# Optimization experiments

Hardware: AMD Instinct MI355X
Metric: run time of the kernel (lower is better)

The kernel has to match this reference:

```python
import jax, jax.numpy as jnp
import numpy as np

BATCH, SEQ, IN, HID = 256, 512, 64, 512


def _xavier(key, shape):
    fan_in, fan_out = shape[1], shape[0]
    limit = float(np.sqrt(6.0 / (fan_in + fan_out)))
    return jax.random.uniform(key, shape, jnp.float32, -limit, limit)


def setup_inputs() -> dict:
    key = jax.random.key(0)
    k1, k2, k3 = jax.random.split(key, 3)
    return {
        "x": jax.random.normal(k1, (BATCH, SEQ, IN), jnp.float32),
        "h0": jnp.zeros((BATCH, HID), jnp.float32),
        "W_ih": _xavier(k2, (HID, IN)),
        "W_hh": _xavier(k3, (HID, HID)),
        "b_ih": jnp.zeros((HID,), jnp.float32),
        "b_hh": jnp.zeros((HID,), jnp.float32),
    }


def reference(x, h0, W_ih, W_hh, b_ih, b_hh):
    # Precompute input projection for all timesteps at once: (B,S,H)
    x_proj = jnp.einsum('bsi,hi->bsh', x, W_ih) + b_ih + b_hh

    def step(h, xp_t):
        h_new = jnp.tanh(xp_t + h @ W_hh.T)  # (B,H)
        return h_new, h_new

    # scan over time axis; xs must be time-major
    h_n, _ = jax.lax.scan(step, h0, jnp.swapaxes(x_proj, 0, 1))
    last_step_features = h_n  # out[:, -1, :] equals final hidden state
    return (last_step_features, h_n)
```

## Files before the change

kernel.cpp:

```cpp
#include <hip/hip_runtime.h>
#include <stdint.h>

#define BATCH 256
#define SEQ   512
#define INDIM 64
#define HID   512

typedef _Float16 half2_t __attribute__((ext_vector_type(2)));

__device__ __forceinline__ float dot2f(uint32_t w, uint32_t h, float acc) {
    return __builtin_amdgcn_fdot2(__builtin_bit_cast(half2_t, w),
                                  __builtin_bit_cast(half2_t, h), acc, false);
}
__device__ __forceinline__ uint32_t pack2(float a, float b) {
    half2_t h; h[0] = (_Float16)a; h[1] = (_Float16)b;
    return __builtin_bit_cast(uint32_t, h);
}
template<int CTRL>
__device__ __forceinline__ float dpp_sum(float x) {
    int xi = __builtin_bit_cast(int, x);
    int yi = __builtin_amdgcn_mov_dpp(xi, CTRL, 0xF, 0xF, true);
    return x + __builtin_bit_cast(float, yi);
}
__device__ __forceinline__ float swz4_sum(float x) {
    int xi = __builtin_bit_cast(int, x);
    int yi = __builtin_amdgcn_ds_swizzle(xi, 0x101F);
    return x + __builtin_bit_cast(float, yi);
}

struct Smem {
    uint4     wl[16][512];
    _Float16  hbuf[2][8][72];
};

#define DOT4(accv, wrow, hc) \
    accv = dot2f((wrow)[0], hc.x, accv); accv = dot2f((wrow)[1], hc.y, accv); \
    accv = dot2f((wrow)[2], hc.z, accv); accv = dot2f((wrow)[3], hc.w, accv);

__global__ __launch_bounds__(512, 2)
void rnn_ksplit_kernel(const float* __restrict__ x,
                       const float* __restrict__ h0,
                       const float* __restrict__ W_ih,
                       const float* __restrict__ W_hh,
                       const float* __restrict__ b_ih,
                       const float* __restrict__ b_hh,
                       float* __restrict__ out)
{
    __shared__ Smem sm;
    const int t = threadIdx.x;
    const int b = blockIdx.x;
    const int s = t & 7;
    const int rbase = t & ~7;

    uint32_t wreg[6][32];
    #pragma unroll
    for (int j = 0; j < 6; ++j) {
        const float* wr = W_hh + (size_t)(rbase + j) * HID + s * 64;
        #pragma unroll
        for (int q = 0; q < 16; ++q) {
            float4 v4 = ((const float4*)wr)[q];
            wreg[j][2*q]   = pack2(v4.x, v4.y);
            wreg[j][2*q+1] = pack2(v4.z, v4.w);
        }
    }
    #pragma unroll
    for (int v = 0; v < 2; ++v) {
        const float* wr = W_hh + (size_t)(rbase + 6 + v) * HID + s * 64;
        #pragma unroll
        for (int c = 0; c < 8; ++c) {
            float4 aa = ((const float4*)wr)[2*c];
            float4 bb = ((const float4*)wr)[2*c+1];
            uint4 wv;
            wv.x = pack2(aa.x, aa.y); wv.y = pack2(aa.z, aa.w);
            wv.z = pack2(bb.x, bb.y); wv.w = pack2(bb.z, bb.w);
            sm.wl[v*8 + c][t] = wv;
        }
    }
    uint32_t wih[8][4];
    #pragma unroll
    for (int j = 0; j < 8; ++j) {
        const float* wr = W_ih + (size_t)(rbase + j) * INDIM + s * 8;
        float4 aa = ((const float4*)wr)[0];
        float4 bb = ((const float4*)wr)[1];
        wih[j][0] = pack2(aa.x, aa.y); wih[j][1] = pack2(aa.z, aa.w);
        wih[j][2] = pack2(bb.x, bb.y); wih[j][3] = pack2(bb.z, bb.w);
    }

    const float bsum = b_ih[t] + b_hh[t];
    sm.hbuf[0][t >> 6][t & 63] = (_Float16)h0[(size_t)b * HID + t];

    const float* xbase = x + (size_t)b * SEQ * INDIM + s * 8;
    float4 xa = ((const float4*)xbase)[0];
    float4 xb = ((const float4*)xbase)[1];

    const bool b0 = (s & 1) != 0, b1 = (s & 2) != 0, b2 = (s & 4) != 0;

    __syncthreads();

    float hlast = 0.f;
    #pragma unroll 1
    for (int tt = 0; tt < SEQ; ++tt) {
        const int tn = (tt + 1 < SEQ) ? tt + 1 : tt;
        const float* xp = xbase + (size_t)tn * INDIM;
        float4 xa_n = ((const float4*)xp)[0];
        float4 xb_n = ((const float4*)xp)[1];

        const int par = tt & 1;
        float a0=0,a1=0,a2=0,a3=0,a4=0,a5=0,a6=0,a7=0;
        const uint4* hp = (const uint4*)&sm.hbuf[par][s][0];

        #pragma unroll
        for (int c = 0; c < 8; ++c) {
            uint4 hc = hp[c];
            uint4 w6 = sm.wl[c][t];
            uint4 w7 = sm.wl[8 + c][t];
            DOT4(a0, &wreg[0][4*c], hc);
            DOT4(a1, &wreg[1][4*c], hc);
            DOT4(a2, &wreg[2][4*c], hc);
            DOT4(a3, &wreg[3][4*c], hc);
            DOT4(a4, &wreg[4][4*c], hc);
            DOT4(a5, &wreg[5][4*c], hc);
            a6 = dot2f(w6.x, hc.x, a6); a6 = dot2f(w6.y, hc.y, a6);
            a6 = dot2f(w6.z, hc.z, a6); a6 = dot2f(w6.w, hc.w, a6);
            a7 = dot2f(w7.x, hc.x, a7); a7 = dot2f(w7.y, hc.y, a7);
            a7 = dot2f(w7.z, hc.z, a7); a7 = dot2f(w7.w, hc.w, a7);
        }

        {
            uint32_t xp0 = pack2(xa.x, xa.y), xp1 = pack2(xa.z, xa.w);
            uint32_t xp2 = pack2(xb.x, xb.y), xp3 = pack2(xb.z, xb.w);
            uint4 xc; xc.x = xp0; xc.y = xp1; xc.z = xp2; xc.w = xp3;
            DOT4(a0, wih[0], xc); DOT4(a1, wih[1], xc);
            DOT4(a2, wih[2], xc); DOT4(a3, wih[3], xc);
            DOT4(a4, wih[4], xc); DOT4(a5, wih[5], xc);
            DOT4(a6, wih[6], xc); DOT4(a7, wih[7], xc);
        }

        float t0 = dpp_sum<0xB1>(a0), u0 = dpp_sum<0xB1>(a1);
        float t1 = dpp_sum<0xB1>(a2), u1 = dpp_sum<0xB1>(a3);
        float t2 = dpp_sum<0xB1>(a4), u2 = dpp_sum<0xB1>(a5);
        float t3 = dpp_sum<0xB1>(a6), u3 = dpp_sum<0xB1>(a7);
        float q0 = b0 ? u0 : t0;
        float q1 = b0 ? u1 : t1;
        float q2 = b0 ? u2 : t2;
        float q3 = b0 ? u3 : t3;
        float r0a = dpp_sum<0x4E>(q0), r0b = dpp_sum<0x4E>(q1);
        float r1a = dpp_sum<0x4E>(q2), r1b = dpp_sum<0x4E>(q3);
        float r0 = b1 ? r0b : r0a;
        float r1 = b1 ? r1b : r1a;
        float f0 = swz4_sum(r0), f1 = swz4_sum(r1);
        float acc = (b2 ? f1 : f0) + bsum;

        float e  = __expf(2.0f * acc);
        float th = 1.0f - 2.0f * __builtin_amdgcn_rcpf(e + 1.0f);

        sm.hbuf[1 - par][t >> 6][t & 63] = (_Float16)th;
        hlast = th;
        xa = xa_n; xb = xb_n;
        __syncthreads();
    }

    out[(size_t)b * HID + t] = hlast;
    out[(size_t)BATCH * HID + (size_t)b * HID + t] = hlast;
}

extern "C" void kernel_launch(void* const* d_in, const int* in_sizes, int n_in,
                              void* d_out, int out_size, void* d_ws, size_t ws_size,
                              hipStream_t stream) {
    (void)in_sizes; (void)n_in; (void)out_size; (void)d_ws; (void)ws_size;
    const float* x    = (const float*)d_in[0];
    const float* h0   = (const float*)d_in[1];
    const float* W_ih = (const float*)d_in[2];
    const float* W_hh = (const float*)d_in[3];
    const float* b_ih = (const float*)d_in[4];
    const float* b_hh = (const float*)d_in[5];
    float* out = (float*)d_out;

    hipLaunchKernelGGL(rnn_ksplit_kernel, dim3(BATCH), dim3(512), 0, stream,
                       x, h0, W_ih, W_hh, b_ih, b_hh, out);
}
```

Before: 962.3 us.

## Rewrite RNN recurrence with MFMA over 16-batch tiles and precomputed input projection

Adds a path that precomputes the input projection for all timesteps with an MFMA GEMM into workspace as fp16. It then runs the recurrence on 16 blocks, each handling 16 batch rows with MFMA 16x16x32. W_hh is split across registers, LDS and a global-memory copy in a pre-swizzled layout. The goal is to replace scalar dot2 work with matrix cores, at the cost of using only 16 CUs, serial latency per step, and a large fp16 workspace. The old kernel remains as a fallback when the workspace is too small.

Measured after the change: 2.628 ms. 173% more time.

```diff
diff --git a/kernel.cpp b/kernel.cpp
--- a/kernel.cpp
+++ b/kernel.cpp
@@ -6,8 +6,222 @@
 #define INDIM 64
 #define HID   512
 
+typedef _Float16 f16;
+typedef _Float16 f16x2 __attribute__((ext_vector_type(2)));
+typedef _Float16 f16x8 __attribute__((ext_vector_type(8)));
+typedef float    f32x4 __attribute__((ext_vector_type(4)));
+
+#define XP_BYTES  134217728ULL
+#define WSC_BYTES 65536ULL
+#define WS_NEED   (XP_BYTES + WSC_BYTES)
+
+__device__ __forceinline__ int row_of(int wv, int rho, int m) {
+    return wv*128 + (rho>>1)*32 + (m>>2)*8 + (rho&1)*4 + (m&3);
+}
+__device__ __forceinline__ f16x2 pkrtz(float a, float b) {
+    return __builtin_bit_cast(f16x2, __builtin_amdgcn_cvt_pkrtz(a, b));
+}
+union FU { f16x8 v; f16x2 h2[4]; uint32_t u[4]; };
+__device__ __forceinline__ f16x8 pack8(float4 a, float4 b) {
+    FU r;
+    r.h2[0] = pkrtz(a.x, a.y); r.h2[1] = pkrtz(a.z, a.w);
+    r.h2[2] = pkrtz(b.x, b.y); r.h2[3] = pkrtz(b.z, b.w);
+    return r.v;
+}
+__device__ __forceinline__ float fast_tanh(float x) {
+    float e = __expf(2.0f * x);
+    return 1.0f - 2.0f * __builtin_amdgcn_rcpf(e + 1.0f);
+}
+__device__ __forceinline__ f32x4 mfma16(f16x8 a, f16x8 b, f32x4 c) {
+    return __builtin_amdgcn_mfma_f32_16x16x32_f16(a, b, c, 0, 0, 0);
+}
+
+__global__ void wconv_kernel(const float* __restrict__ W_hh, f16* __restrict__ wsc)
+{
+    int id = blockIdx.x * 256 + threadIdx.x;
+    if (id >= 2*32*64) return;
+    int l = id & 63, tile = (id >> 6) & 31, ks = id >> 11;
+    int wv = tile >> 3, rho = tile & 7, g = l >> 4, c = l & 15;
+    const float* p = W_hh + (size_t)row_of(wv, rho, c) * HID + (14 + ks) * 32 + g * 8;
+    f16x8 v = pack8(((const float4*)p)[0], ((const float4*)p)[1]);
+    *(f16x8*)(wsc + (size_t)id * 8) = v;
+}
+
+__global__ __launch_bounds__(256)
+void xp_gemm_kernel(const float* __restrict__ x, const float* __restrict__ W_ih,
+                    const float* __restrict__ b_ih, const float* __restrict__ b_hh,
+                    f16* __restrict__ xp)
+{
+    const int t = threadIdx.x, wv = t >> 6, l = t & 63, g = l >> 4, c = l & 15;
+    const int bb = blockIdx.x;
+    const int sc = blockIdx.y;
+
+    f16x8 wf[8][2];
+    #pragma unroll
+    for (int rho = 0; rho < 8; ++rho) {
+        const float* pr = W_ih + (size_t)row_of(wv, rho, c) * INDIM;
+        #pragma unroll
+        for (int kx = 0; kx < 2; ++kx) {
+            const float* p4 = pr + kx * 32 + g * 8;
+            wf[rho][kx] = pack8(((const float4*)p4)[0], ((const float4*)p4)[1]);
+        }
+    }
+    float bias[8][4];
+    #pragma unroll
+    for (int rho = 0; rho < 8; ++rho)
+        #pragma unroll
+        for (int r = 0; r < 4; ++r) {
+            int row = row_of(wv, rho, 4 * g + r);
+            bias[rho][r] = b_ih[row] + b_hh[row];
+        }
+
+    const float* xb = x + (size_t)(bb * 16 + c) * SEQ * INDIM;
+    #pragma unroll 1
+    for (int si = 0; si < 32; ++si) {
+        const int s = sc * 32 + si;
+        const float* xs = xb + (size_t)s * INDIM;
+        f16x8 bx[2];
+        #pragma unroll
+        for (int kx = 0; kx < 2; ++kx) {
+            const float* p4 = xs + kx * 32 + g * 8;
+            bx[kx] = pack8(((const float4*)p4)[0], ((const float4*)p4)[1]);
+        }
+        #pragma unroll
+        for (int rho = 0; rho < 8; ++rho) {
+            f32x4 acc; acc[0] = bias[rho][0]; acc[1] = bias[rho][1];
+            acc[2] = bias[rho][2]; acc[3] = bias[rho][3];
+            acc = mfma16(wf[rho][0], bx[0], acc);
+            acc = mfma16(wf[rho][1], bx[1], acc);
+            f16x2 lo = pkrtz(acc[0], acc[1]), hi = pkrtz(acc[2], acc[3]);
+            uint2 st;
+            st.x = __builtin_bit_cast(uint32_t, lo);
+            st.y = __builtin_bit_cast(uint32_t, hi);
+            size_t idx = (((size_t)bb * SEQ + s) * 32 + wv * 8 + rho) * 64 + l;
+            *(uint2*)(xp + idx * 4) = st;
+        }
+    }
+}
+
+__global__ __launch_bounds__(256, 1)
+void rnn_mfma_kernel(const float* __restrict__ h0, const float* __restrict__ W_hh,
+                     const f16* __restrict__ xp, const f16* __restrict__ wsc,
+                     float* __restrict__ out)
+{
+    __shared__ f16x8 s_wlds[3 * 32 * 64];
+    __shared__ f16x8 s_hbuf[2 * 16 * 64];
+    const int t = threadIdx.x, wv = t >> 6, l = t & 63, g = l >> 4, c = l & 15;
+    const int bb = blockIdx.x;
+
+    f16x8 wreg[11][8];
+    #pragma unroll
+    for (int kk = 0; kk < 11; ++kk)
+        #pragma unroll
+        for (int rho = 0; rho < 8; ++rho) {
+            const float* p4 = W_hh + (size_t)row_of(wv, rho, c) * HID + kk * 32 + g * 8;
+            wreg[kk][rho] = pack8(((const float4*)p4)[0], ((const float4*)p4)[1]);
+        }
+    #pragma unroll
+    for (int kk = 0; kk < 3; ++kk)
+        #pragma unroll
+        for (int rho = 0; rho < 8; ++rho) {
+            const float* p4 = W_hh + (size_t)row_of(wv, rho, c) * HID + (11 + kk) * 32 + g * 8;
+            s_wlds[(kk * 32 + wv * 8 + rho) * 64 + l] =
+                pack8(((const float4*)p4)[0], ((const float4*)p4)[1]);
+        }
+    f16x8 ownf[4];
+    #pragma unroll
+    for (int P = 0; P < 4; ++P) {
+        const float* p4 = h0 + (size_t)(bb * 16 + c) * HID + (4 * wv + P) * 32 + g * 8;
+        ownf[P] = pack8(((const float4*)p4)[0], ((const float4*)p4)[1]);
+        s_hbuf[(4 * wv + P) * 64 + l] = ownf[P];
+    }
+
+    const f16* xpb = xp + ((size_t)bb * SEQ * 32 + wv * 8) * 256;
+    uint2 xn[8];
+    #pragma unroll
+    for (int rho = 0; rho < 8; ++rho)
+        xn[rho] = *(const uint2*)(xpb + rho * 256 + l * 4);
+
+    const f16x8* wsb = (const f16x8*)wsc;
+    __syncthreads();
+
+    int p = 0;
+    #pragma unroll 1
+    for (int tt = 0; tt < SEQ; ++tt) {
+        f16x8 sfA[8];
+        #pragma unroll
+        for (int rho = 0; rho < 8; ++rho)
+            sfA[rho] = wsb[(0 * 32 + wv * 8 + rho) * 64 + l];
+
+        f32x4 acc[8];
+        #pragma unroll
+        for (int rho = 0; rho < 8; ++rho) {
+            f16x2 lo = __builtin_bit_cast(f16x2, xn[rho].x);
+            f16x2 hi = __builtin_bit_cast(f16x2, xn[rho].y);
+            f32x4 a; a[0] = (float)lo[0]; a[1] = (float)lo[1];
+            a[2] = (float)hi[0]; a[3] = (float)hi[1];
+            acc[rho] = a;
+        }
+        if (tt + 1 < SEQ) {
+            const f16* xq = xpb + (size_t)(tt + 1) * 8192;
+            #pragma unroll
+            for (int rho = 0; rho < 8; ++rho)
+                xn[rho] = *(const uint2*)(xq + rho * 256 + l * 4);
+        }
+        const f16x8* hb = s_hbuf + p * 1024;
+
+        #define BFR(KAP) \
+            f16x8 bf; if (((KAP) >> 2) == wv) bf = ownf[(KAP) & 3]; \
+            else bf = hb[(KAP) * 64 + l];
+        #define DOR(KK, KAP) { BFR(KAP); \
+            _Pragma("unroll") for (int rho = 0; rho < 8; ++rho) \
+                acc[rho] = mfma16(wreg[KK][rho], bf, acc[rho]); }
+        #define DOS(SF, KAP) { BFR(KAP); \
+            _Pragma("unroll") for (int rho = 0; rho < 8; ++rho) \
+                acc[rho] = mfma16(SF[rho], bf, acc[rho]); }
+        #define DOL(KKL, KAP) { BFR(KAP); \
+            _Pragma("unroll") for (int rho = 0; rho < 8; ++rho) \
+                acc[rho] = mfma16(s_wlds[((KKL) * 32 + wv * 8 + rho) * 64 + l], bf, acc[rho]); }
+
+        DOR(0, 0); DOR(1, 1); DOR(2, 2); DOR(3, 3); DOR(4, 4); DOR(5, 5);
+        f16x8 sfB[8];
+        #pragma unroll
+        for (int rho = 0; rho < 8; ++rho)
+            sfB[rho] = wsb[(1 * 32 + wv * 8 + rho) * 64 + l];
+        DOS(sfA, 14);
+        DOR(6, 6); DOR(7, 7); DOR(8, 8); DOR(9, 9); DOR(10, 10);
+        DOS(sfB, 15);
+        DOL(0, 11); DOL(1, 12); DOL(2, 13);
+
+        f16x8* hw = s_hbuf + (1 - p) * 1024;
+        #pragma unroll
+        for (int P = 0; P < 4; ++P) {
+            float t0 = fast_tanh(acc[2*P][0]),   t1 = fast_tanh(acc[2*P][1]);
+            float t2 = fast_tanh(acc[2*P][2]),   t3 = fast_tanh(acc[2*P][3]);
+            float t4 = fast_tanh(acc[2*P+1][0]), t5 = fast_tanh(acc[2*P+1][1]);
+            float t6 = fast_tanh(acc[2*P+1][2]), t7 = fast_tanh(acc[2*P+1][3]);
+            FU fu;
+            fu.h2[0] = pkrtz(t0, t1); fu.h2[1] = pkrtz(t2, t3);
+            fu.h2[2] = pkrtz(t4, t5); fu.h2[3] = pkrtz(t6, t7);
+            ownf[P] = fu.v;
+            hw[(4 * wv + P) * 64 + l] = fu.v;
+            if (tt == SEQ - 1) {
+                float* ob = out + (size_t)(bb * 16 + c) * HID;
+                float* o2 = ob + (size_t)BATCH * HID;
+                int ra = row_of(wv, 2 * P, 4 * g);
+                int rb = row_of(wv, 2 * P + 1, 4 * g);
+                ob[ra + 0] = t0; ob[ra + 1] = t1; ob[ra + 2] = t2; ob[ra + 3] = t3;
+                ob[rb + 0] = t4; ob[rb + 1] = t5; ob[rb + 2] = t6; ob[rb + 3] = t7;
+                o2[ra + 0] = t0; o2[ra + 1] = t1; o2[ra + 2] = t2; o2[ra + 3] = t3;
+                o2[rb + 0] = t4; o2[rb + 1] = t5; o2[rb + 2] = t6; o2[rb + 3] = t7;
+            }
+        }
+        __syncthreads();
+        p ^= 1;
+    }
+}
+
 typedef _Float16 half2_t __attribute__((ext_vector_type(2)));
-
 __device__ __forceinline__ float dot2f(uint32_t w, uint32_t h, float acc) {
     return __builtin_amdgcn_fdot2(__builtin_bit_cast(half2_t, w),
                                   __builtin_bit_cast(half2_t, h), acc, false);
@@ -27,26 +241,21 @@
     int yi = __builtin_amdgcn_ds_swizzle(xi, 0x101F);
     return x + __builtin_bit_cast(float, yi);
 }
-
-struct Smem {
+struct SmemFB {
     uint4     wl[16][512];
     _Float16  hbuf[2][8][72];
 };
-
-#define DOT4(accv, wrow, hc) \
+#define FB_DOT4(accv, wrow, hc) \
     accv = dot2f((wrow)[0], hc.x, accv); accv = dot2f((wrow)[1], hc.y, accv); \
     accv = dot2f((wrow)[2], hc.z, accv); accv = dot2f((wrow)[3], hc.w, accv);
 
 __global__ __launch_bounds__(512, 2)
-void rnn_ksplit_kernel(const float* __restrict__ x,
-                       const float* __restrict__ h0,
-                       const float* __restrict__ W_ih,
-                       const float* __restrict__ W_hh,
-                       const float* __restrict__ b_ih,
-                       const float* __restrict__ b_hh,
+void rnn_ksplit_kernel(const float* __restrict__ x, const float* __restrict__ h0,
+                       const float* __restrict__ W_ih, const float* __restrict__ W_hh,
+                       const float* __restrict__ b_ih, const float* __restrict__ b_hh,
                        float* __restrict__ out)
 {
-    __shared__ Smem sm;
+    __shared__ SmemFB sm;
     const int t = threadIdx.x;
     const int b = blockIdx.x;
     const int s = t & 7;
@@ -67,13 +276,13 @@
     for (int v = 0; v < 2; ++v) {
         const float* wr = W_hh + (size_t)(rbase + 6 + v) * HID + s * 64;
         #pragma unroll
-        for (int c = 0; c < 8; ++c) {
-            float4 aa = ((const float4*)wr)[2*c];
-            float4 bb = ((const float4*)wr)[2*c+1];
-            uint4 wv;
-            wv.x = pack2(aa.x, aa.y); wv.y = pack2(aa.z, aa.w);
-            wv.z = pack2(bb.x, bb.y); wv.w = pack2(bb.z, bb.w);
-            sm.wl[v*8 + c][t] = wv;
+        for (int cc = 0; cc < 8; ++cc) {
+            float4 aa = ((const float4*)wr)[2*cc];
+            float4 bb2 = ((const float4*)wr)[2*cc+1];
+            uint4 wv2;
+            wv2.x = pack2(aa.x, aa.y); wv2.y = pack2(aa.z, aa.w);
+            wv2.z = pack2(bb2.x, bb2.y); wv2.w = pack2(bb2.z, bb2.w);
+            sm.wl[v*8 + cc][t] = wv2;
         }
     }
     uint32_t wih[8][4];
@@ -81,61 +290,53 @@
     for (int j = 0; j < 8; ++j) {
         const float* wr = W_ih + (size_t)(rbase + j) * INDIM + s * 8;
         float4 aa = ((const float4*)wr)[0];
-        float4 bb = ((const float4*)wr)[1];
+        float4 bb2 = ((const float4*)wr)[1];
         wih[j][0] = pack2(aa.x, aa.y); wih[j][1] = pack2(aa.z, aa.w);
-        wih[j][2] = pack2(bb.x, bb.y); wih[j][3] = pack2(bb.z, bb.w);
-    }
-
+        wih[j][2] = pack2(bb2.x, bb2.y); wih[j][3] = pack2(bb2.z, bb2.w);
+    }
     const float bsum = b_ih[t] + b_hh[t];
     sm.hbuf[0][t >> 6][t & 63] = (_Float16)h0[(size_t)b * HID + t];
-
     const float* xbase = x + (size_t)b * SEQ * INDIM + s * 8;
     float4 xa = ((const float4*)xbase)[0];
     float4 xb = ((const float4*)xbase)[1];
-
     const bool b0 = (s & 1) != 0, b1 = (s & 2) != 0, b2 = (s & 4) != 0;
-
     __syncthreads();
 
     float hlast = 0.f;
     #pragma unroll 1
     for (int tt = 0; tt < SEQ; ++tt) {
         const int tn = (tt + 1 < SEQ) ? tt + 1 : tt;
-        const float* xp = xbase + (size_t)tn * INDIM;
-        float4 xa_n = ((const float4*)xp)[0];
-        float4 xb_n = ((const float4*)xp)[1];
-
+        const float* xpf = xbase + (size_t)tn * INDIM;
+        float4 xa_n = ((const float4*)xpf)[0];
+        float4 xb_n = ((const float4*)xpf)[1];
         const int par = tt & 1;
         float a0=0,a1=0,a2=0,a3=0,a4=0,a5=0,a6=0,a7=0;
         const uint4* hp = (const uint4*)&sm.hbuf[par][s][0];
-
-        #pragma unroll
-        for (int c = 0; c < 8; ++c) {
-            uint4 hc = hp[c];
-            uint4 w6 = sm.wl[c][t];
-            uint4 w7 = sm.wl[8 + c][t];
-            DOT4(a0, &wreg[0][4*c], hc);
-            DOT4(a1, &wreg[1][4*c], hc);
-            DOT4(a2, &wreg[2][4*c], hc);
-            DOT4(a3, &wreg[3][4*c], hc);
-            DOT4(a4, &wreg[4][4*c], hc);
-            DOT4(a5, &wreg[5][4*c], hc);
+        #pragma unroll
+        for (int cc = 0; cc < 8; ++cc) {
+            uint4 hc = hp[cc];
+            uint4 w6 = sm.wl[cc][t];
+            uint4 w7 = sm.wl[8 + cc][t];
+            FB_DOT4(a0, &wreg[0][4*cc], hc);
+            FB_DOT4(a1, &wreg[1][4*cc], hc);
+            FB_DOT4(a2, &wreg[2][4*cc], hc);
+            FB_DOT4(a3, &wreg[3][4*cc], hc);
+            FB_DOT4(a4, &wreg[4][4*cc], hc);
+            FB_DOT4(a5, &wreg[5][4*cc], hc);
             a6 = dot2f(w6.x, hc.x, a6); a6 = dot2f(w6.y, hc.y, a6);
             a6 = dot2f(w6.z, hc.z, a6); a6 = dot2f(w6.w, hc.w, a6);
             a7 = dot2f(w7.x, hc.x, a7); a7 = dot2f(w7.y, hc.y, a7);
             a7 = dot2f(w7.z, hc.z, a7); a7 = dot2f(w7.w, hc.w, a7);
         }
-
         {
             uint32_t xp0 = pack2(xa.x, xa.y), xp1 = pack2(xa.z, xa.w);
             uint32_t xp2 = pack2(xb.x, xb.y), xp3 = pack2(xb.z, xb.w);
             uint4 xc; xc.x = xp0; xc.y = xp1; xc.z = xp2; xc.w = xp3;
-            DOT4(a0, wih[0], xc); DOT4(a1, wih[1], xc);
-            DOT4(a2, wih[2], xc); DOT4(a3, wih[3], xc);
-            DOT4(a4, wih[4], xc); DOT4(a5, wih[5], xc);
-            DOT4(a6, wih[6], xc); DOT4(a7, wih[7], xc);
-        }
-
+            FB_DOT4(a0, wih[0], xc); FB_DOT4(a1, wih[1], xc);
+            FB_DOT4(a2, wih[2], xc); FB_DOT4(a3, wih[3], xc);
+            FB_DOT4(a4, wih[4], xc); FB_DOT4(a5, wih[5], xc);
+            FB_DOT4(a6, wih[6], xc); FB_DOT4(a7, wih[7], xc);
+        }
         float t0 = dpp_sum<0xB1>(a0), u0 = dpp_sum<0xB1>(a1);
         float t1 = dpp_sum<0xB1>(a2), u1 = dpp_sum<0xB1>(a3);
         float t2 = dpp_sum<0xB1>(a4), u2 = dpp_sum<0xB1>(a5);
@@ -149,17 +350,14 @@
         float r0 = b1 ? r0b : r0a;
         float r1 = b1 ? r1b : r1a;
         float f0 = swz4_sum(r0), f1 = swz4_sum(r1);
-        float acc = (b2 ? f1 : f0) + bsum;
-
-        float e  = __expf(2.0f * acc);
+        float accv = (b2 ? f1 : f0) + bsum;
+        float e  = __expf(2.0f * accv);
         float th = 1.0f - 2.0f * __builtin_amdgcn_rcpf(e + 1.0f);
-
         sm.hbuf[1 - par][t >> 6][t & 63] = (_Float16)th;
         hlast = th;
         xa = xa_n; xb = xb_n;
         __syncthreads();
     }
-
     out[(size_t)b * HID + t] = hlast;
     out[(size_t)BATCH * HID + (size_t)b * HID + t] = hlast;
 }
@@ -167,7 +365,7 @@
 extern "C" void kernel_launch(void* const* d_in, const int* in_sizes, int n_in,
                               void* d_out, int out_size, void* d_ws, size_t ws_size,
                               hipStream_t stream) {
-    (void)in_sizes; (void)n_in; (void)out_size; (void)d_ws; (void)ws_size;
+    (void)in_sizes; (void)n_in; (void)out_size;
     const float* x    = (const float*)d_in[0];
     const float* h0   = (const float*)d_in[1];
     const float* W_ih = (const float*)d_in[2];
@@ -176,6 +374,16 @@
     const float* b_hh = (const float*)d_in[5];
     float* out = (float*)d_out;
 
-    hipLaunchKernelGGL(rnn_ksplit_kernel, dim3(BATCH), dim3(512), 0, stream,
-                       x, h0, W_ih, W_hh, b_ih, b_hh, out);
-}
+    if (ws_size >= WS_NEED) {
+        f16* xp  = (f16*)d_ws;
+        f16* wsc = (f16*)((char*)d_ws + XP_BYTES);
+        hipLaunchKernelGGL(wconv_kernel, dim3(16), dim3(256), 0, stream, W_hh, wsc);
+        hipLaunchKernelGGL(xp_gemm_kernel, dim3(16, 16), dim3(256), 0, stream,
+                           x, W_ih, b_ih, b_hh, xp);
+        hipLaunchKernelGGL(rnn_mfma_kernel, dim3(16), dim3(256), 0, stream,
+                           h0, W_hh, xp, wsc, out);
+    } else {
+        hipLaunchKernelGGL(rnn_ksplit_kernel, dim3(BATCH), dim3(512), 0, stream,
+                           x, h0, W_ih, W_hh, b_ih, b_hh, out);
+    }
+}
```
